# Kernel tuning notes

Measured on AMD Instinct MI355X. Metric: run time of the kernel, lower is better.

The kernel has to match this reference:

```python
import jax, jax.numpy as jnp
import numpy as np

NUM_GRAPHS = 64
NEG_SLOPE = 0.2  # DGL GATConv default negative_slope


def _gat_layer(h, W, a_l, a_r, b, src, dst, n_nodes):
    # DGL GATConv, num_heads=1: feat = h @ W (no bias in fc),
    # e_ij = LeakyReLU(a_l . feat_src + a_r . feat_dst), softmax over incoming
    # edges of each dst node, out_dst = sum alpha * feat_src + bias.
    feat = h @ W                      # [N, D]
    el = feat @ a_l                   # [N]
    er = feat @ a_r                   # [N]
    e = jax.nn.leaky_relu(el[src] + er[dst], NEG_SLOPE)   # [E]
    m = jax.ops.segment_max(e, dst, num_segments=n_nodes)  # per-dst max
    ex = jnp.exp(e - m[dst])
    s = jax.ops.segment_sum(ex, dst, num_segments=n_nodes)
    alpha = ex / s[dst]               # edge softmax
    out = jax.ops.segment_sum(feat[src] * alpha[:, None], dst, num_segments=n_nodes)
    return out + b


def setup_inputs() -> dict:
    key = jax.random.key(0)
    ks = jax.random.split(key, 12)
    N, E, D_IN, D_H, C = 100000, 1600000, 128, 128, 2
    h = jax.random.normal(ks[0], (N, D_IN), dtype=jnp.float32)
    src = jax.random.randint(ks[1], (E,), 0, N)
    dst = jax.random.randint(ks[2], (E,), 0, N)
    graph_id = jnp.sort(jax.random.randint(ks[3], (N,), 0, NUM_GRAPHS))
    sc = 1.0 / np.sqrt(D_IN)
    params = {
        'W1': jax.random.normal(ks[4], (D_IN, D_H), dtype=jnp.float32) * sc,
        'al1': jax.random.normal(ks[5], (D_H,), dtype=jnp.float32) * sc,
        'ar1': jax.random.normal(ks[6], (D_H,), dtype=jnp.float32) * sc,
        'b1': jnp.zeros((D_H,), dtype=jnp.float32),
        'W2': jax.random.normal(ks[7], (D_H, D_H), dtype=jnp.float32) * sc,
        'al2': jax.random.normal(ks[8], (D_H,), dtype=jnp.float32) * sc,
        'ar2': jax.random.normal(ks[9], (D_H,), dtype=jnp.float32) * sc,
        'b2': jnp.zeros((D_H,), dtype=jnp.float32),
        'Wfc': jax.random.normal(ks[10], (D_H, C), dtype=jnp.float32) * sc,
        'bfc': jnp.zeros((C,), dtype=jnp.float32),
    }
    return dict(h=h, src=src, dst=dst, graph_id=graph_id, **params)


def reference(h, src, dst, graph_id, W1, al1, ar1, b1, W2, al2, ar2, b2, Wfc, bfc):
    n_nodes = h.shape[0]
    x = jax.nn.relu(_gat_layer(h, W1, al1, ar1, b1, src, dst, n_nodes))
    x = jax.nn.relu(_gat_layer(x, W2, al2, ar2, b2, src, dst, n_nodes))
    # dgl.mean_nodes over the batched graph
    counts = jax.ops.segment_sum(jnp.ones((n_nodes,), x.dtype), graph_id,
                                 num_segments=NUM_GRAPHS)
    hg = jax.ops.segment_sum(x, graph_id, num_segments=NUM_GRAPHS)
    hg = hg / jnp.clip(counts, 1.0)[:, None]          # [G, D]
    logits = hg @ Wfc + bfc                            # [G, C]
    return jax.nn.log_softmax(logits, axis=-1)
```

## Files before the change

kernel.cpp:

```cpp
#include <hip/hip_runtime.h>
#include <math.h>

#define NUM_GRAPHS 64
#define D 128
#define PCHUNK 16
#define MT 64
#define ETILE 4096

typedef __attribute__((ext_vector_type(8))) short bf16x8;
typedef __attribute__((ext_vector_type(4))) float f32x4;
typedef __attribute__((ext_vector_type(2))) float f32x2;

__device__ __forceinline__ unsigned bf16rne(float x) {
    unsigned u = __float_as_uint(x);
    return (u + 0x7fffu + ((u >> 16) & 1u)) >> 16;
}
__device__ __forceinline__ float bflo(unsigned u) { return __uint_as_float(u << 16); }
__device__ __forceinline__ float bfhi(unsigned u) { return __uint_as_float(u & 0xffff0000u); }

__device__ __forceinline__ unsigned encf(float f) {
    unsigned u = __float_as_uint(f);
    return (u & 0x80000000u) ? ~u : (u | 0x80000000u);
}
__device__ __forceinline__ float decf(unsigned e) {
    unsigned u = (e & 0x80000000u) ? (e & 0x7fffffffu) : ~e;
    return __uint_as_float(u);
}


__global__ __launch_bounds__(256) void k_front(
    const int* __restrict__ dst, int* __restrict__ bhist, int E, int nbT,
    const float* __restrict__ W1, const float* __restrict__ W2,
    unsigned short* __restrict__ Wt1, unsigned short* __restrict__ Wt2,
    const int* __restrict__ gid, int* __restrict__ gs, int* __restrict__ ge, int N) {
    __shared__ int h[1024];
    int b = blockIdx.x;
    int tid = threadIdx.x;
    if (b < nbT) {
        for (int i = tid; i < 1024; i += 256) h[i] = 0;
        __syncthreads();
        int e0 = b * ETILE;
        int e1 = min(e0 + ETILE, E);
        for (int i = e0 + tid; i < e1; i += 256) atomicAdd(&h[dst[i] >> 7], 1);
        __syncthreads();
        for (int i = tid; i < 1024; i += 256)
            if (h[i]) atomicAdd(&bhist[i], h[i]);
    } else if (b < nbT + 16) {
        int bb = b - nbT;
        const float* W = (bb & 8) ? W2 : W1;
        unsigned short* Wt = (bb & 8) ? Wt2 : Wt1;
        int n = (bb & 7) * 16 + (tid >> 4);
        int c = tid & 15;
        unsigned v[8];
        #pragma unroll
        for (int j = 0; j < 8; ++j) v[j] = bf16rne(W[(c * 8 + j) * D + n]);
        uint4 pk;
        pk.x = v[0] | (v[1] << 16);
        pk.y = v[2] | (v[3] << 16);
        pk.z = v[4] | (v[5] << 16);
        pk.w = v[6] | (v[7] << 16);
        ((uint4*)Wt)[n * 16 + c] = pk;
    } else {
        int n = (b - nbT - 16) * 256 + tid;
        if (n >= N) return;
        int g = gid[n];
        if (n == 0 || gid[n - 1] != g) gs[g] = n;
        if (n == N - 1 || gid[n + 1] != g) ge[g] = n;
    }
}

__global__ __launch_bounds__(1024) void k_bucket_scan(const int* __restrict__ bhist,
                                                      int* __restrict__ bbase,
                                                      int* __restrict__ bcur,
                                                      int NB, int E,
                                                      int* __restrict__ row_ptr, int N) {
    __shared__ int sm[1024];
    int t = threadIdx.x;
    int v = (t < NB) ? bhist[t] : 0;
    sm[t] = v;
    __syncthreads();
    for (int off = 1; off < 1024; off <<= 1) {
        int y = (t >= off) ? sm[t - off] : 0;
        __syncthreads();
        sm[t] += y;
        __syncthreads();
    }
    if (t < NB) { bbase[t] = sm[t] - v; bcur[t] = sm[t] - v; }
    if (t == 0) { bbase[NB] = E; row_ptr[N] = E; }
}

__global__ __launch_bounds__(256) void k_partition(const int* __restrict__ src,
                                                   const int* __restrict__ dst,
                                                   int* __restrict__ bcur,
                                                   unsigned* __restrict__ part, int E) {
    __shared__ int h[1024];
    __shared__ int cur[1024];
    int tid = threadIdx.x;
    for (int i = tid; i < 1024; i += 256) h[i] = 0;
    __syncthreads();
    int e0 = blockIdx.x * ETILE;
    int e1 = min(e0 + ETILE, E);
    for (int i = e0 + tid; i < e1; i += 256) atomicAdd(&h[dst[i] >> 7], 1);
    __syncthreads();
    for (int i = tid; i < 1024; i += 256) {
        int c = h[i];
        cur[i] = c ? atomicAdd(&bcur[i], c) : 0;
    }
    __syncthreads();
    for (int i = e0 + tid; i < e1; i += 256) {
        int d = dst[i];
        int b = d >> 7;
        int pos = atomicAdd(&cur[b], 1);
        part[pos] = (unsigned)src[i] | ((unsigned)(d & 127) << 17);
    }
}


__global__ __launch_bounds__(256) void k_gemm_mfma_sort(
    const void* __restrict__ Xv, int x_fp32,
    const unsigned short* __restrict__ Wt16,
    const float* __restrict__ al, const float* __restrict__ ar,
    unsigned short* __restrict__ feat16, float* __restrict__ el,
    float* __restrict__ er, unsigned* __restrict__ glmax_u, int N, int gemmBlocks,
    const unsigned* __restrict__ part, const int* __restrict__ bbase,
    int* __restrict__ row_ptr, int* __restrict__ csr_src) {
    __shared__ uint4 WsU[128 * 16];
    __shared__ uint4 XsU[MT * 16];
    __shared__ float smax[4];
    int bx = blockIdx.x;
    int T = gridDim.x;
    int g0 = (int)((long long)bx * gemmBlocks / T);
    int g1 = (int)((long long)(bx + 1) * gemmBlocks / T);
    int tid = threadIdx.x;

    if (g1 == g0) {
        int b = bx - g0;
        int base = bbase[b];
        int bcnt = bbase[b + 1] - base;
        int* ldeg = (int*)XsU;
        int* lcur = ldeg + 128;
        if (tid < 128) ldeg[tid] = 0;
        __syncthreads();
        for (int i = tid; i < bcnt; i += 256)
            atomicAdd(&ldeg[part[base + i] >> 17], 1);
        __syncthreads();
        int myv = (tid < 128) ? ldeg[tid] : 0;
        for (int off = 1; off < 128; off <<= 1) {
            int y = 0;
            if (tid < 128 && tid >= off) y = ldeg[tid - off];
            __syncthreads();
            if (tid < 128) ldeg[tid] += y;
            __syncthreads();
        }
        if (tid < 128) {
            int excl = ldeg[tid] - myv;
            int node = (b << 7) + tid;
            if (node < N) row_ptr[node] = base + excl;
            lcur[tid] = base + excl;
        }
        __syncthreads();
        for (int i = tid; i < bcnt; i += 256) {
            unsigned v = part[base + i];
            int pos = atomicAdd(&lcur[v >> 17], 1);
            csr_src[pos] = (int)(v & 0x1FFFFu);
        }
        return;
    }

    int row0 = g0 * MT;

    for (int idx = tid; idx < 128 * 16; idx += 256) {
        int n = idx >> 4, c = idx & 15;
        WsU[(n << 4) | (c ^ (n & 15))] = ((const uint4*)Wt16)[idx];
    }
    if (x_fp32) {
        const float4* X4 = (const float4*)Xv;
        for (int idx = tid; idx < MT * 16; idx += 256) {
            int n = idx >> 4, c = idx & 15;
            int row = row0 + n;
            uint4 o = make_uint4(0, 0, 0, 0);
            if (row < N) {
                float4 f0 = X4[(size_t)row * 32 + c * 2];
                float4 f1 = X4[(size_t)row * 32 + c * 2 + 1];
                o.x = bf16rne(f0.x) | (bf16rne(f0.y) << 16);
                o.y = bf16rne(f0.z) | (bf16rne(f0.w) << 16);
                o.z = bf16rne(f1.x) | (bf16rne(f1.y) << 16);
                o.w = bf16rne(f1.z) | (bf16rne(f1.w) << 16);
            }
            XsU[(n << 4) | (c ^ (n & 15))] = o;
        }
    } else {
        const uint4* X16 = (const uint4*)Xv;
        for (int idx = tid; idx < MT * 16; idx += 256) {
            int n = idx >> 4, c = idx & 15;
            int row = row0 + n;
            uint4 o = make_uint4(0, 0, 0, 0);
            if (row < N) o = X16[(size_t)row * 16 + c];
            XsU[(n << 4) | (c ^ (n & 15))] = o;
        }
    }
    __syncthreads();

    int lane = tid & 63, w = tid >> 6;
    int quad = lane >> 4, l16 = lane & 15;
    const bf16x8* WsF = (const bf16x8*)WsU;
    const bf16x8* XsF = (const bf16x8*)XsU;
    f32x4 acc[8];
    #pragma unroll
    for (int i = 0; i < 8; ++i) acc[i] = (f32x4){0.f, 0.f, 0.f, 0.f};

    int arow = w * 16 + l16;
    #pragma unroll
    for (int ks = 0; ks < 4; ++ks) {
        int c = ks * 4 + quad;
        bf16x8 A = XsF[(arow << 4) | (c ^ l16)];
        #pragma unroll
        for (int nt = 0; nt < 8; ++nt) {
            bf16x8 B = WsF[((nt * 16 + l16) << 4) | (c ^ l16)];
            acc[nt] = __builtin_amdgcn_mfma_f32_16x16x32_bf16(A, B, acc[nt], 0, 0, 0);
        }
    }

    float alv[8], arv[8];
    #pragma unroll
    for (int nt = 0; nt < 8; ++nt) { alv[nt] = al[nt * 16 + l16]; arv[nt] = ar[nt * 16 + l16]; }
    float lmax = -1e30f;
    #pragma unroll
    for (int r = 0; r < 4; ++r) {
        float pl = 0.f, pr = 0.f;
        #pragma unroll
        for (int nt = 0; nt < 8; ++nt) { pl += acc[nt][r] * alv[nt]; pr += acc[nt][r] * arv[nt]; }
        #pragma unroll
        for (int o = 1; o < 16; o <<= 1) { pl += __shfl_xor(pl, o); pr += __shfl_xor(pr, o); }
        int row = row0 + w * 16 + quad * 4 + r;
        if (l16 == 0 && row < N) { el[row] = pl; er[row] = pr; }
        lmax = fmaxf(lmax, pl);
    }
    lmax = fmaxf(lmax, __shfl_xor(lmax, 16));
    lmax = fmaxf(lmax, __shfl_xor(lmax, 32));
    if (lane == 0) smax[w] = lmax;

    unsigned short* XsS = (unsigned short*)XsU;
    #pragma unroll
    for (int nt = 0; nt < 8; ++nt)
        #pragma unroll
        for (int r = 0; r < 4; ++r) {
            int lrow = w * 16 + quad * 4 + r;
            int col = nt * 16 + l16;
            int ch = col >> 3;
            int sc = ch ^ (lrow & 15);
            XsS[lrow * 128 + sc * 8 + (col & 7)] = (unsigned short)bf16rne(acc[nt][r]);
        }
    __syncthreads();
    if (tid == 0) {
        float bm = fmaxf(fmaxf(smax[0], smax[1]), fmaxf(smax[2], smax[3]));
        atomicMax(glmax_u, encf(bm));
    }
    for (int idx = tid; idx < MT * 16; idx += 256) {
        int n = idx >> 4, c = idx & 15;
        int row = row0 + n;
        if (row < N) ((uint4*)feat16)[(size_t)row * 16 + c] = XsU[(n << 4) | (c ^ (n & 15))];
    }
}


__global__ __launch_bounds__(256) void k_aggregate(
    const unsigned short* __restrict__ feat16, const float* __restrict__ el,
    const float* __restrict__ er, const int* __restrict__ row_ptr,
    const int* __restrict__ csr_src, const float* __restrict__ bias,
    const unsigned* __restrict__ glmax_u, unsigned short* __restrict__ outv, int N) {
    int wid = (blockIdx.x * blockDim.x + threadIdx.x) >> 6;
    int lane = threadIdx.x & 63;
    if (wid >= N) return;
    int beg = row_ptr[wid], end = row_ptr[wid + 1];
    float erd = er[wid];
    float M = decf(glmax_u[0]) + erd;
    M = fmaxf(M, 0.2f * M);

    int qa = lane >> 4, sub = lane & 15;
    const char* fb = (const char*)feat16 + (sub << 4);
    f32x2 a0 = {0.f, 0.f}, a1 = {0.f, 0.f}, a2 = {0.f, 0.f}, a3 = {0.f, 0.f};
    float s = 0.f;
    int j = beg + qa;
    for (; j + 12 < end; j += 16) {
        int sn0 = csr_src[j], sn1 = csr_src[j + 4];
        int sn2 = csr_src[j + 8], sn3 = csr_src[j + 12];
        float t0 = el[sn0] + erd, t1 = el[sn1] + erd;
        float t2 = el[sn2] + erd, t3 = el[sn3] + erd;
        uint4 q0 = *(const uint4*)(fb + ((unsigned)sn0 << 8));
        uint4 q1 = *(const uint4*)(fb + ((unsigned)sn1 << 8));
        uint4 q2 = *(const uint4*)(fb + ((unsigned)sn2 << 8));
        uint4 q3 = *(const uint4*)(fb + ((unsigned)sn3 << 8));
        t0 = fmaxf(t0, 0.2f * t0); t1 = fmaxf(t1, 0.2f * t1);
        t2 = fmaxf(t2, 0.2f * t2); t3 = fmaxf(t3, 0.2f * t3);
        float w0 = __expf(t0 - M), w1 = __expf(t1 - M);
        float w2 = __expf(t2 - M), w3 = __expf(t3 - M);
        s += (w0 + w1) + (w2 + w3);
        f32x2 f;
        f.x = bflo(q0.x); f.y = bfhi(q0.x); a0 += w0 * f;
        f.x = bflo(q0.y); f.y = bfhi(q0.y); a1 += w0 * f;
        f.x = bflo(q0.z); f.y = bfhi(q0.z); a2 += w0 * f;
        f.x = bflo(q0.w); f.y = bfhi(q0.w); a3 += w0 * f;
        f.x = bflo(q1.x); f.y = bfhi(q1.x); a0 += w1 * f;
        f.x = bflo(q1.y); f.y = bfhi(q1.y); a1 += w1 * f;
        f.x = bflo(q1.z); f.y = bfhi(q1.z); a2 += w1 * f;
        f.x = bflo(q1.w); f.y = bfhi(q1.w); a3 += w1 * f;
        f.x = bflo(q2.x); f.y = bfhi(q2.x); a0 += w2 * f;
        f.x = bflo(q2.y); f.y = bfhi(q2.y); a1 += w2 * f;
        f.x = bflo(q2.z); f.y = bfhi(q2.z); a2 += w2 * f;
        f.x = bflo(q2.w); f.y = bfhi(q2.w); a3 += w2 * f;
        f.x = bflo(q3.x); f.y = bfhi(q3.x); a0 += w3 * f;
        f.x = bflo(q3.y); f.y = bfhi(q3.y); a1 += w3 * f;
        f.x = bflo(q3.z); f.y = bfhi(q3.z); a2 += w3 * f;
        f.x = bflo(q3.w); f.y = bfhi(q3.w); a3 += w3 * f;
    }
    for (; j + 4 < end; j += 8) {
        int sn0 = csr_src[j], sn1 = csr_src[j + 4];
        float t0 = el[sn0] + erd, t1 = el[sn1] + erd;
        uint4 q0 = *(const uint4*)(fb + ((unsigned)sn0 << 8));
        uint4 q1 = *(const uint4*)(fb + ((unsigned)sn1 << 8));
        t0 = fmaxf(t0, 0.2f * t0); t1 = fmaxf(t1, 0.2f * t1);
        float w0 = __expf(t0 - M), w1 = __expf(t1 - M);
        s += w0 + w1;
        f32x2 f;
        f.x = bflo(q0.x); f.y = bfhi(q0.x); a0 += w0 * f;
        f.x = bflo(q0.y); f.y = bfhi(q0.y); a1 += w0 * f;
        f.x = bflo(q0.z); f.y = bfhi(q0.z); a2 += w0 * f;
        f.x = bflo(q0.w); f.y = bfhi(q0.w); a3 += w0 * f;
        f.x = bflo(q1.x); f.y = bfhi(q1.x); a0 += w1 * f;
        f.x = bflo(q1.y); f.y = bfhi(q1.y); a1 += w1 * f;
        f.x = bflo(q1.z); f.y = bfhi(q1.z); a2 += w1 * f;
        f.x = bflo(q1.w); f.y = bfhi(q1.w); a3 += w1 * f;
    }
    if (j < end) {
        int sn = csr_src[j];
        float t = el[sn] + erd;
        uint4 q = *(const uint4*)(fb + ((unsigned)sn << 8));
        t = fmaxf(t, 0.2f * t);
        float w = __expf(t - M);
        s += w;
        f32x2 f;
        f.x = bflo(q.x); f.y = bfhi(q.x); a0 += w * f;
        f.x = bflo(q.y); f.y = bfhi(q.y); a1 += w * f;
        f.x = bflo(q.z); f.y = bfhi(q.z); a2 += w * f;
        f.x = bflo(q.w); f.y = bfhi(q.w); a3 += w * f;
    }
    float vr[8] = {a0.x, a0.y, a1.x, a1.y, a2.x, a2.y, a3.x, a3.y};
    #pragma unroll
    for (int c = 0; c < 8; ++c) {
        vr[c] += __shfl_xor(vr[c], 16);
        vr[c] += __shfl_xor(vr[c], 32);
    }
    s += __shfl_xor(s, 16);
    s += __shfl_xor(s, 32);
    float inv = (end > beg) ? 1.f / s : 0.f;
    if (lane < 16) {
        float4 b0 = ((const float4*)bias)[lane * 2];
        float4 b1 = ((const float4*)bias)[lane * 2 + 1];
        float v[8];
        v[0] = fmaxf(vr[0] * inv + b0.x, 0.f);
        v[1] = fmaxf(vr[1] * inv + b0.y, 0.f);
        v[2] = fmaxf(vr[2] * inv + b0.z, 0.f);
        v[3] = fmaxf(vr[3] * inv + b0.w, 0.f);
        v[4] = fmaxf(vr[4] * inv + b1.x, 0.f);
        v[5] = fmaxf(vr[5] * inv + b1.y, 0.f);
        v[6] = fmaxf(vr[6] * inv + b1.z, 0.f);
        v[7] = fmaxf(vr[7] * inv + b1.w, 0.f);
        uint4 pk;
        pk.x = bf16rne(v[0]) | (bf16rne(v[1]) << 16);
        pk.y = bf16rne(v[2]) | (bf16rne(v[3]) << 16);
        pk.z = bf16rne(v[4]) | (bf16rne(v[5]) << 16);
        pk.w = bf16rne(v[6]) | (bf16rne(v[7]) << 16);
        ((uint4*)outv)[(size_t)wid * 16 + lane] = pk;
    }
}


__global__ __launch_bounds__(256) void k_pool_partial(const unsigned short* __restrict__ x,
                                                      const int* __restrict__ gs,
                                                      const int* __restrict__ ge,
                                                      float* __restrict__ hg) {
    int g = blockIdx.x, c = blockIdx.y;
    int start = gs[g], last = ge[g];
    if (start > last) return;
    int sub = threadIdx.x & 15;
    int r   = threadIdx.x >> 4;
    const uint4* x4 = (const uint4*)x;
    float acc[8] = {};
    for (int n = start + c * 16 + r; n <= last; n += PCHUNK * 16) {
        uint4 q = x4[(size_t)n * 16 + sub];
        acc[0] += bflo(q.x); acc[1] += bfhi(q.x);
        acc[2] += bflo(q.y); acc[3] += bfhi(q.y);
        acc[4] += bflo(q.z); acc[5] += bfhi(q.z);
        acc[6] += bflo(q.w); acc[7] += bfhi(q.w);
    }
    __shared__ float sm[256][8];
    #pragma unroll
    for (int k = 0; k < 8; ++k) sm[threadIdx.x][k] = acc[k];
    __syncthreads();
    for (int off = 8; off >= 1; off >>= 1) {
        if (r < off) {
            #pragma unroll
            for (int k = 0; k < 8; ++k)
                sm[threadIdx.x][k] += sm[threadIdx.x + off * 16][k];
        }
        __syncthreads();
    }
    if (r == 0) {
        #pragma unroll
        for (int k = 0; k < 8; ++k)
            atomicAdd(&hg[g * D + sub * 8 + k], sm[sub][k]);
    }
}

__global__ void k_final(const float* __restrict__ hg, const int* __restrict__ gs,
                        const int* __restrict__ ge, const float* __restrict__ Wfc,
                        const float* __restrict__ bfc, float* __restrict__ out) {
    int g = threadIdx.x;
    if (g >= NUM_GRAPHS) return;
    int start = gs[g], last = ge[g];
    float cnt = (start <= last) ? (float)(last - start + 1) : 1.f;
    float ic = 1.f / cnt;
    float l0 = bfc[0], l1 = bfc[1];
    for (int d = 0; d < D; d++) {
        float v = hg[g * D + d] * ic;
        l0 += v * Wfc[2 * d];
        l1 += v * Wfc[2 * d + 1];
    }
    float mm = fmaxf(l0, l1);
    float lse = mm + logf(expf(l0 - mm) + expf(l1 - mm));
    out[2 * g] = l0 - lse;
    out[2 * g + 1] = l1 - lse;
}


extern "C" void kernel_launch(void* const* d_in, const int* in_sizes, int n_in,
                              void* d_out, int out_size, void* d_ws, size_t ws_size,
                              hipStream_t stream) {
    const float* h   = (const float*)d_in[0];
    const int* src   = (const int*)d_in[1];
    const int* dst   = (const int*)d_in[2];
    const int* gid   = (const int*)d_in[3];
    const float* W1  = (const float*)d_in[4];
    const float* al1 = (const float*)d_in[5];
    const float* ar1 = (const float*)d_in[6];
    const float* b1  = (const float*)d_in[7];
    const float* W2  = (const float*)d_in[8];
    const float* al2 = (const float*)d_in[9];
    const float* ar2 = (const float*)d_in[10];
    const float* b2  = (const float*)d_in[11];
    const float* Wfc = (const float*)d_in[12];
    const float* bfc = (const float*)d_in[13];
    float* out = (float*)d_out;

    int N = in_sizes[0] / D;
    int E = in_sizes[1];
    int NB = (N + 127) >> 7;

    char* p = (char*)d_ws;
    unsigned short* feat16  = (unsigned short*)p; p += (size_t)N * D * 2;
    unsigned short* featAgg = (unsigned short*)p; p += (size_t)N * D * 2;
    float* el    = (float*)p; p += (size_t)N * 4;
    float* er    = (float*)p; p += (size_t)N * 4;
    int* row_ptr = (int*)p;   p += (size_t)(N + 4) * 4;
    int* csr_src = (int*)p;   p += (size_t)E * 4;
    unsigned* part = (unsigned*)p; p += (size_t)E * 4;
    int* bhist   = (int*)p;   p += 1028 * 4;
    unsigned* glmaxu = (unsigned*)p; p += 4 * 4;
    float* hg    = (float*)p; p += NUM_GRAPHS * D * 4;
    size_t zbytes = (char*)p - (char*)bhist;
    int* bbase   = (int*)p;   p += 1028 * 4;
    int* bcur    = (int*)p;   p += 1028 * 4;
    int* gs      = (int*)p;   p += NUM_GRAPHS * 4;
    int* ge      = (int*)p;   p += NUM_GRAPHS * 4;
    unsigned short* Wt1 = (unsigned short*)p; p += D * D * 2;
    unsigned short* Wt2 = (unsigned short*)p; p += D * D * 2;

    int nbN = (N + 255) / 256;
    int nbW = (N * 64 + 255) / 256;
    int nbT = (E + ETILE - 1) / ETILE;
    int gemmB = (N + MT - 1) / MT;

    hipMemsetAsync(bhist, 0, zbytes, stream);
    hipMemsetAsync(gs, 0x7f, NUM_GRAPHS * 4, stream);
    hipMemsetAsync(ge, 0xff, NUM_GRAPHS * 4, stream);

    k_front<<<nbT + 16 + nbN, 256, 0, stream>>>(dst, bhist, E, nbT,
                                                W1, W2, Wt1, Wt2, gid, gs, ge, N);
    k_bucket_scan<<<1, 1024, 0, stream>>>(bhist, bbase, bcur, NB, E, row_ptr, N);
    k_partition<<<nbT, 256, 0, stream>>>(src, dst, bcur, part, E);

    k_gemm_mfma_sort<<<gemmB + NB, 256, 0, stream>>>(
        h, 1, Wt1, al1, ar1, feat16, el, er, glmaxu, N, gemmB,
        part, bbase, row_ptr, csr_src);
    k_aggregate<<<nbW, 256, 0, stream>>>(feat16, el, er, row_ptr, csr_src,
                                         b1, glmaxu, featAgg, N);

    k_gemm_mfma_sort<<<gemmB, 256, 0, stream>>>(
        featAgg, 0, Wt2, al2, ar2, feat16, el, er, glmaxu + 1, N, gemmB,
        part, bbase, row_ptr, csr_src);
    k_aggregate<<<nbW, 256, 0, stream>>>(feat16, el, er, row_ptr, csr_src,
                                         b2, glmaxu + 1, featAgg, N);

    k_pool_partial<<<dim3(NUM_GRAPHS, PCHUNK), 256, 0, stream>>>(featAgg, gs, ge, hg);
    k_final<<<1, 64, 0, stream>>>(hg, gs, ge, Wfc, bfc, out);
}
```

Measured before the change: 355.9 us.

## Precompute edge softmax weights and inverse sums in a separate per-bucket kernel

Adds a k_weights kernel that computes the exp attention weight for each edge in CSR order into a buffer, and accumulates per-destination inverse sums with shared-memory atomics, once per 128-node bucket. The aggregate kernel then reads these precomputed weights instead of gathering el and running exp per edge, and the csr array now stores packed src|dst-local values. The aim is to take the random el gather and transcendental work out of the latency-bound gather loop. In exchange it adds an extra kernel launch and an extra E-sized write and read of the weight buffer per layer. The shared-atomic summation order also differs from the previous per-lane sums.

```diff
diff --git a/kernel.cpp b/kernel.cpp
--- a/kernel.cpp
+++ b/kernel.cpp
@@ -123,7 +123,7 @@
     unsigned short* __restrict__ feat16, float* __restrict__ el,
     float* __restrict__ er, unsigned* __restrict__ glmax_u, int N, int gemmBlocks,
     const unsigned* __restrict__ part, const int* __restrict__ bbase,
-    int* __restrict__ row_ptr, int* __restrict__ csr_src) {
+    int* __restrict__ row_ptr, unsigned* __restrict__ csr_src) {
     __shared__ uint4 WsU[128 * 16];
     __shared__ uint4 XsU[MT * 16];
     __shared__ float smax[4];
@@ -162,7 +162,7 @@
         for (int i = tid; i < bcnt; i += 256) {
             unsigned v = part[base + i];
             int pos = atomicAdd(&lcur[v >> 17], 1);
-            csr_src[pos] = (int)(v & 0x1FFFFu);
+            csr_src[pos] = v;
         }
         return;
     }
@@ -264,38 +264,64 @@
 }
 
 
+__global__ __launch_bounds__(256) void k_weights(
+    const unsigned* __restrict__ csr_packed, const int* __restrict__ bbase,
+    const float* __restrict__ el, const float* __restrict__ er,
+    const unsigned* __restrict__ glmax_u, float* __restrict__ wbuf,
+    float* __restrict__ sinv, int N) {
+    __shared__ float sl[128];
+    int b = blockIdx.x;
+    int base = bbase[b], endq = bbase[b + 1];
+    int tid = threadIdx.x;
+    if (tid < 128) sl[tid] = 0.f;
+    __syncthreads();
+    float EL = decf(glmax_u[0]);
+    for (int i = base + tid; i < endq; i += 256) {
+        unsigned v = csr_packed[i];
+        int sn = v & 0x1FFFFu;
+        int dl = v >> 17;
+        float erd = er[(b << 7) + dl];
+        float M = EL + erd; M = fmaxf(M, 0.2f * M);
+        float t = el[sn] + erd; t = fmaxf(t, 0.2f * t);
+        float w = __expf(t - M);
+        wbuf[i] = w;
+        atomicAdd(&sl[dl], w);
+    }
+    __syncthreads();
+    if (tid < 128) {
+        int node = (b << 7) + tid;
+        if (node < N) {
+            float s = sl[tid];
+            sinv[node] = s > 0.f ? 1.f / s : 0.f;
+        }
+    }
+}
+
+
 __global__ __launch_bounds__(256) void k_aggregate(
-    const unsigned short* __restrict__ feat16, const float* __restrict__ el,
-    const float* __restrict__ er, const int* __restrict__ row_ptr,
-    const int* __restrict__ csr_src, const float* __restrict__ bias,
-    const unsigned* __restrict__ glmax_u, unsigned short* __restrict__ outv, int N) {
+    const unsigned short* __restrict__ feat16,
+    const unsigned* __restrict__ csr_packed, const float* __restrict__ wbuf,
+    const float* __restrict__ sinv, const int* __restrict__ row_ptr,
+    const float* __restrict__ bias, unsigned short* __restrict__ outv, int N) {
     int wid = (blockIdx.x * blockDim.x + threadIdx.x) >> 6;
     int lane = threadIdx.x & 63;
     if (wid >= N) return;
     int beg = row_ptr[wid], end = row_ptr[wid + 1];
-    float erd = er[wid];
-    float M = decf(glmax_u[0]) + erd;
-    M = fmaxf(M, 0.2f * M);
+    float si = sinv[wid];
 
     int qa = lane >> 4, sub = lane & 15;
     const char* fb = (const char*)feat16 + (sub << 4);
     f32x2 a0 = {0.f, 0.f}, a1 = {0.f, 0.f}, a2 = {0.f, 0.f}, a3 = {0.f, 0.f};
-    float s = 0.f;
     int j = beg + qa;
     for (; j + 12 < end; j += 16) {
-        int sn0 = csr_src[j], sn1 = csr_src[j + 4];
-        int sn2 = csr_src[j + 8], sn3 = csr_src[j + 12];
-        float t0 = el[sn0] + erd, t1 = el[sn1] + erd;
-        float t2 = el[sn2] + erd, t3 = el[sn3] + erd;
-        uint4 q0 = *(const uint4*)(fb + ((unsigned)sn0 << 8));
-        uint4 q1 = *(const uint4*)(fb + ((unsigned)sn1 << 8));
-        uint4 q2 = *(const uint4*)(fb + ((unsigned)sn2 << 8));
-        uint4 q3 = *(const uint4*)(fb + ((unsigned)sn3 << 8));
-        t0 = fmaxf(t0, 0.2f * t0); t1 = fmaxf(t1, 0.2f * t1);
-        t2 = fmaxf(t2, 0.2f * t2); t3 = fmaxf(t3, 0.2f * t3);
-        float w0 = __expf(t0 - M), w1 = __expf(t1 - M);
-        float w2 = __expf(t2 - M), w3 = __expf(t3 - M);
-        s += (w0 + w1) + (w2 + w3);
+        unsigned v0 = csr_packed[j], v1 = csr_packed[j + 4];
+        unsigned v2 = csr_packed[j + 8], v3 = csr_packed[j + 12];
+        float w0 = wbuf[j], w1 = wbuf[j + 4];
+        float w2 = wbuf[j + 8], w3 = wbuf[j + 12];
+        uint4 q0 = *(const uint4*)(fb + ((v0 & 0x1FFFFu) << 8));
+        uint4 q1 = *(const uint4*)(fb + ((v1 & 0x1FFFFu) << 8));
+        uint4 q2 = *(const uint4*)(fb + ((v2 & 0x1FFFFu) << 8));
+        uint4 q3 = *(const uint4*)(fb + ((v3 & 0x1FFFFu) << 8));
         f32x2 f;
         f.x = bflo(q0.x); f.y = bfhi(q0.x); a0 += w0 * f;
         f.x = bflo(q0.y); f.y = bfhi(q0.y); a1 += w0 * f;
@@ -314,31 +340,10 @@
         f.x = bflo(q3.z); f.y = bfhi(q3.z); a2 += w3 * f;
         f.x = bflo(q3.w); f.y = bfhi(q3.w); a3 += w3 * f;
     }
-    for (; j + 4 < end; j += 8) {
-        int sn0 = csr_src[j], sn1 = csr_src[j + 4];
-        float t0 = el[sn0] + erd, t1 = el[sn1] + erd;
-        uint4 q0 = *(const uint4*)(fb + ((unsigned)sn0 << 8));
-        uint4 q1 = *(const uint4*)(fb + ((unsigned)sn1 << 8));
-        t0 = fmaxf(t0, 0.2f * t0); t1 = fmaxf(t1, 0.2f * t1);
-        float w0 = __expf(t0 - M), w1 = __expf(t1 - M);
-        s += w0 + w1;
-        f32x2 f;
-        f.x = bflo(q0.x); f.y = bfhi(q0.x); a0 += w0 * f;
-        f.x = bflo(q0.y); f.y = bfhi(q0.y); a1 += w0 * f;
-        f.x = bflo(q0.z); f.y = bfhi(q0.z); a2 += w0 * f;
-        f.x = bflo(q0.w); f.y = bfhi(q0.w); a3 += w0 * f;
-        f.x = bflo(q1.x); f.y = bfhi(q1.x); a0 += w1 * f;
-        f.x = bflo(q1.y); f.y = bfhi(q1.y); a1 += w1 * f;
-        f.x = bflo(q1.z); f.y = bfhi(q1.z); a2 += w1 * f;
-        f.x = bflo(q1.w); f.y = bfhi(q1.w); a3 += w1 * f;
-    }
-    if (j < end) {
-        int sn = csr_src[j];
-        float t = el[sn] + erd;
-        uint4 q = *(const uint4*)(fb + ((unsigned)sn << 8));
-        t = fmaxf(t, 0.2f * t);
-        float w = __expf(t - M);
-        s += w;
+    for (; j < end; j += 4) {
+        unsigned v = csr_packed[j];
+        float w = wbuf[j];
+        uint4 q = *(const uint4*)(fb + ((v & 0x1FFFFu) << 8));
         f32x2 f;
         f.x = bflo(q.x); f.y = bfhi(q.x); a0 += w * f;
         f.x = bflo(q.y); f.y = bfhi(q.y); a1 += w * f;
@@ -351,21 +356,18 @@
         vr[c] += __shfl_xor(vr[c], 16);
         vr[c] += __shfl_xor(vr[c], 32);
     }
-    s += __shfl_xor(s, 16);
-    s += __shfl_xor(s, 32);
-    float inv = (end > beg) ? 1.f / s : 0.f;
     if (lane < 16) {
         float4 b0 = ((const float4*)bias)[lane * 2];
         float4 b1 = ((const float4*)bias)[lane * 2 + 1];
         float v[8];
-        v[0] = fmaxf(vr[0] * inv + b0.x, 0.f);
-        v[1] = fmaxf(vr[1] * inv + b0.y, 0.f);
-        v[2] = fmaxf(vr[2] * inv + b0.z, 0.f);
-        v[3] = fmaxf(vr[3] * inv + b0.w, 0.f);
-        v[4] = fmaxf(vr[4] * inv + b1.x, 0.f);
-        v[5] = fmaxf(vr[5] * inv + b1.y, 0.f);
-        v[6] = fmaxf(vr[6] * inv + b1.z, 0.f);
-        v[7] = fmaxf(vr[7] * inv + b1.w, 0.f);
+        v[0] = fmaxf(vr[0] * si + b0.x, 0.f);
+        v[1] = fmaxf(vr[1] * si + b0.y, 0.f);
+        v[2] = fmaxf(vr[2] * si + b0.z, 0.f);
+        v[3] = fmaxf(vr[3] * si + b0.w, 0.f);
+        v[4] = fmaxf(vr[4] * si + b1.x, 0.f);
+        v[5] = fmaxf(vr[5] * si + b1.y, 0.f);
+        v[6] = fmaxf(vr[6] * si + b1.z, 0.f);
+        v[7] = fmaxf(vr[7] * si + b1.w, 0.f);
         uint4 pk;
         pk.x = bf16rne(v[0]) | (bf16rne(v[1]) << 16);
         pk.y = bf16rne(v[2]) | (bf16rne(v[3]) << 16);
@@ -462,9 +464,11 @@
     unsigned short* featAgg = (unsigned short*)p; p += (size_t)N * D * 2;
     float* el    = (float*)p; p += (size_t)N * 4;
     float* er    = (float*)p; p += (size_t)N * 4;
+    float* sinv  = (float*)p; p += (size_t)N * 4;
     int* row_ptr = (int*)p;   p += (size_t)(N + 4) * 4;
-    int* csr_src = (int*)p;   p += (size_t)E * 4;
+    unsigned* csr_src = (unsigned*)p; p += (size_t)E * 4;
     unsigned* part = (unsigned*)p; p += (size_t)E * 4;
+    float* wbuf  = (float*)p; p += (size_t)E * 4;
     int* bhist   = (int*)p;   p += 1028 * 4;
     unsigned* glmaxu = (unsigned*)p; p += 4 * 4;
     float* hg    = (float*)p; p += NUM_GRAPHS * D * 4;
@@ -493,14 +497,16 @@
     k_gemm_mfma_sort<<<gemmB + NB, 256, 0, stream>>>(
         h, 1, Wt1, al1, ar1, feat16, el, er, glmaxu, N, gemmB,
         part, bbase, row_ptr, csr_src);
-    k_aggregate<<<nbW, 256, 0, stream>>>(feat16, el, er, row_ptr, csr_src,
-                                         b1, glmaxu, featAgg, N);
+    k_weights<<<NB, 256, 0, stream>>>(csr_src, bbase, el, er, glmaxu, wbuf, sinv, N);
+    k_aggregate<<<nbW, 256, 0, stream>>>(feat16, csr_src, wbuf, sinv, row_ptr,
+                                         b1, featAgg, N);
 
     k_gemm_mfma_sort<<<gemmB, 256, 0, stream>>>(
         featAgg, 0, Wt2, al2, ar2, feat16, el, er, glmaxu + 1, N, gemmB,
         part, bbase, row_ptr, csr_src);
-    k_aggregate<<<nbW, 256, 0, stream>>>(feat16, el, er, row_ptr, csr_src,
-                                         b2, glmaxu + 1, featAgg, N);
+    k_weights<<<NB, 256, 0, stream>>>(csr_src, bbase, el, er, glmaxu + 1, wbuf, sinv, N);
+    k_aggregate<<<nbW, 256, 0, stream>>>(feat16, csr_src, wbuf, sinv, row_ptr,
+                                         b2, featAgg, N);
 
     k_pool_partial<<<dim3(NUM_GRAPHS, PCHUNK), 256, 0, stream>>>(featAgg, gs, ge, hg);
     k_final<<<1, 64, 0, stream>>>(hg, gs, ge, Wfc, bfc, out);
```

Result: slower. 392.9 us (+10.4%).

## Fuse mean-node pooling into second GAT aggregation with replicated atomic accumulators

Applied to the files above, without the earlier changes.

The second aggregate kernel now scales each node's output by the inverse node count of its graph. It reduces the four nodes of a block in shared memory and atomically adds the result into one of 16 replicated per-graph accumulators, instead of writing bf16 features and running a separate pooling kernel. Inverse counts are computed in the scan kernel, and the final kernel sums the replicas before the classifier. This removes a full feature write and re-read plus one launch, at the cost of many global float atomics with possible contention on sorted graph ids.

```diff
diff --git a/kernel.cpp b/kernel.cpp
--- a/kernel.cpp
+++ b/kernel.cpp
@@ -3,9 +3,9 @@
 
 #define NUM_GRAPHS 64
 #define D 128
-#define PCHUNK 16
 #define MT 64
 #define ETILE 4096
+#define NREP 16
 
 typedef __attribute__((ext_vector_type(8))) short bf16x8;
 typedef __attribute__((ext_vector_type(4))) float f32x4;
@@ -73,7 +73,10 @@
                                                       int* __restrict__ bbase,
                                                       int* __restrict__ bcur,
                                                       int NB, int E,
-                                                      int* __restrict__ row_ptr, int N) {
+                                                      int* __restrict__ row_ptr, int N,
+                                                      const int* __restrict__ gs,
+                                                      const int* __restrict__ ge,
+                                                      float* __restrict__ ginv) {
     __shared__ int sm[1024];
     int t = threadIdx.x;
     int v = (t < NB) ? bhist[t] : 0;
@@ -87,6 +90,10 @@
     }
     if (t < NB) { bbase[t] = sm[t] - v; bcur[t] = sm[t] - v; }
     if (t == 0) { bbase[NB] = E; row_ptr[N] = E; }
+    if (t < NUM_GRAPHS) {
+        int s = gs[t], e = ge[t];
+        ginv[t] = (s <= e) ? 1.f / (float)(e - s + 1) : 0.f;
+    }
 }
 
 __global__ __launch_bounds__(256) void k_partition(const int* __restrict__ src,
@@ -264,173 +271,187 @@
 }
 
 
+template <bool POOL>
 __global__ __launch_bounds__(256) void k_aggregate(
     const unsigned short* __restrict__ feat16, const float* __restrict__ el,
     const float* __restrict__ er, const int* __restrict__ row_ptr,
     const int* __restrict__ csr_src, const float* __restrict__ bias,
-    const unsigned* __restrict__ glmax_u, unsigned short* __restrict__ outv, int N) {
-    int wid = (blockIdx.x * blockDim.x + threadIdx.x) >> 6;
-    int lane = threadIdx.x & 63;
-    if (wid >= N) return;
-    int beg = row_ptr[wid], end = row_ptr[wid + 1];
-    float erd = er[wid];
-    float M = decf(glmax_u[0]) + erd;
-    M = fmaxf(M, 0.2f * M);
-
-    int qa = lane >> 4, sub = lane & 15;
-    const char* fb = (const char*)feat16 + (sub << 4);
-    f32x2 a0 = {0.f, 0.f}, a1 = {0.f, 0.f}, a2 = {0.f, 0.f}, a3 = {0.f, 0.f};
-    float s = 0.f;
-    int j = beg + qa;
-    for (; j + 12 < end; j += 16) {
-        int sn0 = csr_src[j], sn1 = csr_src[j + 4];
-        int sn2 = csr_src[j + 8], sn3 = csr_src[j + 12];
-        float t0 = el[sn0] + erd, t1 = el[sn1] + erd;
-        float t2 = el[sn2] + erd, t3 = el[sn3] + erd;
-        uint4 q0 = *(const uint4*)(fb + ((unsigned)sn0 << 8));
-        uint4 q1 = *(const uint4*)(fb + ((unsigned)sn1 << 8));
-        uint4 q2 = *(const uint4*)(fb + ((unsigned)sn2 << 8));
-        uint4 q3 = *(const uint4*)(fb + ((unsigned)sn3 << 8));
-        t0 = fmaxf(t0, 0.2f * t0); t1 = fmaxf(t1, 0.2f * t1);
-        t2 = fmaxf(t2, 0.2f * t2); t3 = fmaxf(t3, 0.2f * t3);
-        float w0 = __expf(t0 - M), w1 = __expf(t1 - M);
-        float w2 = __expf(t2 - M), w3 = __expf(t3 - M);
-        s += (w0 + w1) + (w2 + w3);
-        f32x2 f;
-        f.x = bflo(q0.x); f.y = bfhi(q0.x); a0 += w0 * f;
-        f.x = bflo(q0.y); f.y = bfhi(q0.y); a1 += w0 * f;
-        f.x = bflo(q0.z); f.y = bfhi(q0.z); a2 += w0 * f;
-        f.x = bflo(q0.w); f.y = bfhi(q0.w); a3 += w0 * f;
-        f.x = bflo(q1.x); f.y = bfhi(q1.x); a0 += w1 * f;
-        f.x = bflo(q1.y); f.y = bfhi(q1.y); a1 += w1 * f;
-        f.x = bflo(q1.z); f.y = bfhi(q1.z); a2 += w1 * f;
-        f.x = bflo(q1.w); f.y = bfhi(q1.w); a3 += w1 * f;
-        f.x = bflo(q2.x); f.y = bfhi(q2.x); a0 += w2 * f;
-        f.x = bflo(q2.y); f.y = bfhi(q2.y); a1 += w2 * f;
-        f.x = bflo(q2.z); f.y = bfhi(q2.z); a2 += w2 * f;
-        f.x = bflo(q2.w); f.y = bfhi(q2.w); a3 += w2 * f;
-        f.x = bflo(q3.x); f.y = bfhi(q3.x); a0 += w3 * f;
-        f.x = bflo(q3.y); f.y = bfhi(q3.y); a1 += w3 * f;
-        f.x = bflo(q3.z); f.y = bfhi(q3.z); a2 += w3 * f;
-        f.x = bflo(q3.w); f.y = bfhi(q3.w); a3 += w3 * f;
-    }
-    for (; j + 4 < end; j += 8) {
-        int sn0 = csr_src[j], sn1 = csr_src[j + 4];
-        float t0 = el[sn0] + erd, t1 = el[sn1] + erd;
-        uint4 q0 = *(const uint4*)(fb + ((unsigned)sn0 << 8));
-        uint4 q1 = *(const uint4*)(fb + ((unsigned)sn1 << 8));
-        t0 = fmaxf(t0, 0.2f * t0); t1 = fmaxf(t1, 0.2f * t1);
-        float w0 = __expf(t0 - M), w1 = __expf(t1 - M);
-        s += w0 + w1;
-        f32x2 f;
-        f.x = bflo(q0.x); f.y = bfhi(q0.x); a0 += w0 * f;
-        f.x = bflo(q0.y); f.y = bfhi(q0.y); a1 += w0 * f;
-        f.x = bflo(q0.z); f.y = bfhi(q0.z); a2 += w0 * f;
-        f.x = bflo(q0.w); f.y = bfhi(q0.w); a3 += w0 * f;
-        f.x = bflo(q1.x); f.y = bfhi(q1.x); a0 += w1 * f;
-        f.x = bflo(q1.y); f.y = bfhi(q1.y); a1 += w1 * f;
-        f.x = bflo(q1.z); f.y = bfhi(q1.z); a2 += w1 * f;
-        f.x = bflo(q1.w); f.y = bfhi(q1.w); a3 += w1 * f;
-    }
-    if (j < end) {
-        int sn = csr_src[j];
-        float t = el[sn] + erd;
-        uint4 q = *(const uint4*)(fb + ((unsigned)sn << 8));
-        t = fmaxf(t, 0.2f * t);
-        float w = __expf(t - M);
-        s += w;
-        f32x2 f;
-        f.x = bflo(q.x); f.y = bfhi(q.x); a0 += w * f;
-        f.x = bflo(q.y); f.y = bfhi(q.y); a1 += w * f;
-        f.x = bflo(q.z); f.y = bfhi(q.z); a2 += w * f;
-        f.x = bflo(q.w); f.y = bfhi(q.w); a3 += w * f;
-    }
-    float vr[8] = {a0.x, a0.y, a1.x, a1.y, a2.x, a2.y, a3.x, a3.y};
-    #pragma unroll
-    for (int c = 0; c < 8; ++c) {
-        vr[c] += __shfl_xor(vr[c], 16);
-        vr[c] += __shfl_xor(vr[c], 32);
-    }
-    s += __shfl_xor(s, 16);
-    s += __shfl_xor(s, 32);
-    float inv = (end > beg) ? 1.f / s : 0.f;
-    if (lane < 16) {
-        float4 b0 = ((const float4*)bias)[lane * 2];
-        float4 b1 = ((const float4*)bias)[lane * 2 + 1];
-        float v[8];
-        v[0] = fmaxf(vr[0] * inv + b0.x, 0.f);
-        v[1] = fmaxf(vr[1] * inv + b0.y, 0.f);
-        v[2] = fmaxf(vr[2] * inv + b0.z, 0.f);
-        v[3] = fmaxf(vr[3] * inv + b0.w, 0.f);
-        v[4] = fmaxf(vr[4] * inv + b1.x, 0.f);
-        v[5] = fmaxf(vr[5] * inv + b1.y, 0.f);
-        v[6] = fmaxf(vr[6] * inv + b1.z, 0.f);
-        v[7] = fmaxf(vr[7] * inv + b1.w, 0.f);
-        uint4 pk;
-        pk.x = bf16rne(v[0]) | (bf16rne(v[1]) << 16);
-        pk.y = bf16rne(v[2]) | (bf16rne(v[3]) << 16);
-        pk.z = bf16rne(v[4]) | (bf16rne(v[5]) << 16);
-        pk.w = bf16rne(v[6]) | (bf16rne(v[7]) << 16);
-        ((uint4*)outv)[(size_t)wid * 16 + lane] = pk;
-    }
-}
-
-
-__global__ __launch_bounds__(256) void k_pool_partial(const unsigned short* __restrict__ x,
-                                                      const int* __restrict__ gs,
-                                                      const int* __restrict__ ge,
-                                                      float* __restrict__ hg) {
-    int g = blockIdx.x, c = blockIdx.y;
-    int start = gs[g], last = ge[g];
-    if (start > last) return;
-    int sub = threadIdx.x & 15;
-    int r   = threadIdx.x >> 4;
-    const uint4* x4 = (const uint4*)x;
-    float acc[8] = {};
-    for (int n = start + c * 16 + r; n <= last; n += PCHUNK * 16) {
-        uint4 q = x4[(size_t)n * 16 + sub];
-        acc[0] += bflo(q.x); acc[1] += bfhi(q.x);
-        acc[2] += bflo(q.y); acc[3] += bfhi(q.y);
-        acc[4] += bflo(q.z); acc[5] += bfhi(q.z);
-        acc[6] += bflo(q.w); acc[7] += bfhi(q.w);
-    }
-    __shared__ float sm[256][8];
-    #pragma unroll
-    for (int k = 0; k < 8; ++k) sm[threadIdx.x][k] = acc[k];
-    __syncthreads();
-    for (int off = 8; off >= 1; off >>= 1) {
-        if (r < off) {
+    const unsigned* __restrict__ glmax_u, unsigned short* __restrict__ outv,
+    const int* __restrict__ gid, const float* __restrict__ ginv,
+    float* __restrict__ hgrep, int N) {
+    int tid = threadIdx.x;
+    int wid = (blockIdx.x * blockDim.x + tid) >> 6;
+    int lane = tid & 63;
+    int w = tid >> 6;
+    bool active = wid < N;
+    if (!POOL && !active) return;
+
+    float v[8];
+    int g = 0;
+    float ic = 0.f;
+    if (active) {
+        int beg = row_ptr[wid], end = row_ptr[wid + 1];
+        float erd = er[wid];
+        float M = decf(glmax_u[0]) + erd;
+        M = fmaxf(M, 0.2f * M);
+
+        int qa = lane >> 4, sub = lane & 15;
+        const char* fb = (const char*)feat16 + (sub << 4);
+        f32x2 a0 = {0.f, 0.f}, a1 = {0.f, 0.f}, a2 = {0.f, 0.f}, a3 = {0.f, 0.f};
+        float s = 0.f;
+        int j = beg + qa;
+        for (; j + 12 < end; j += 16) {
+            int sn0 = csr_src[j], sn1 = csr_src[j + 4];
+            int sn2 = csr_src[j + 8], sn3 = csr_src[j + 12];
+            float t0 = el[sn0] + erd, t1 = el[sn1] + erd;
+            float t2 = el[sn2] + erd, t3 = el[sn3] + erd;
+            uint4 q0 = *(const uint4*)(fb + ((unsigned)sn0 << 8));
+            uint4 q1 = *(const uint4*)(fb + ((unsigned)sn1 << 8));
+            uint4 q2 = *(const uint4*)(fb + ((unsigned)sn2 << 8));
+            uint4 q3 = *(const uint4*)(fb + ((unsigned)sn3 << 8));
+            t0 = fmaxf(t0, 0.2f * t0); t1 = fmaxf(t1, 0.2f * t1);
+            t2 = fmaxf(t2, 0.2f * t2); t3 = fmaxf(t3, 0.2f * t3);
+            float w0 = __expf(t0 - M), w1 = __expf(t1 - M);
+            float w2 = __expf(t2 - M), w3 = __expf(t3 - M);
+            s += (w0 + w1) + (w2 + w3);
+            f32x2 f;
+            f.x = bflo(q0.x); f.y = bfhi(q0.x); a0 += w0 * f;
+            f.x = bflo(q0.y); f.y = bfhi(q0.y); a1 += w0 * f;
+            f.x = bflo(q0.z); f.y = bfhi(q0.z); a2 += w0 * f;
+            f.x = bflo(q0.w); f.y = bfhi(q0.w); a3 += w0 * f;
+            f.x = bflo(q1.x); f.y = bfhi(q1.x); a0 += w1 * f;
+            f.x = bflo(q1.y); f.y = bfhi(q1.y); a1 += w1 * f;
+            f.x = bflo(q1.z); f.y = bfhi(q1.z); a2 += w1 * f;
+            f.x = bflo(q1.w); f.y = bfhi(q1.w); a3 += w1 * f;
+            f.x = bflo(q2.x); f.y = bfhi(q2.x); a0 += w2 * f;
+            f.x = bflo(q2.y); f.y = bfhi(q2.y); a1 += w2 * f;
+            f.x = bflo(q2.z); f.y = bfhi(q2.z); a2 += w2 * f;
+            f.x = bflo(q2.w); f.y = bfhi(q2.w); a3 += w2 * f;
+            f.x = bflo(q3.x); f.y = bfhi(q3.x); a0 += w3 * f;
+            f.x = bflo(q3.y); f.y = bfhi(q3.y); a1 += w3 * f;
+            f.x = bflo(q3.z); f.y = bfhi(q3.z); a2 += w3 * f;
+            f.x = bflo(q3.w); f.y = bfhi(q3.w); a3 += w3 * f;
+        }
+        for (; j + 4 < end; j += 8) {
+            int sn0 = csr_src[j], sn1 = csr_src[j + 4];
+            float t0 = el[sn0] + erd, t1 = el[sn1] + erd;
+            uint4 q0 = *(const uint4*)(fb + ((unsigned)sn0 << 8));
+            uint4 q1 = *(const uint4*)(fb + ((unsigned)sn1 << 8));
+            t0 = fmaxf(t0, 0.2f * t0); t1 = fmaxf(t1, 0.2f * t1);
+            float w0 = __expf(t0 - M), w1 = __expf(t1 - M);
+            s += w0 + w1;
+            f32x2 f;
+            f.x = bflo(q0.x); f.y = bfhi(q0.x); a0 += w0 * f;
+            f.x = bflo(q0.y); f.y = bfhi(q0.y); a1 += w0 * f;
+            f.x = bflo(q0.z); f.y = bfhi(q0.z); a2 += w0 * f;
+            f.x = bflo(q0.w); f.y = bfhi(q0.w); a3 += w0 * f;
+            f.x = bflo(q1.x); f.y = bfhi(q1.x); a0 += w1 * f;
+            f.x = bflo(q1.y); f.y = bfhi(q1.y); a1 += w1 * f;
+            f.x = bflo(q1.z); f.y = bfhi(q1.z); a2 += w1 * f;
+            f.x = bflo(q1.w); f.y = bfhi(q1.w); a3 += w1 * f;
+        }
+        if (j < end) {
+            int sn = csr_src[j];
+            float t = el[sn] + erd;
+            uint4 q = *(const uint4*)(fb + ((unsigned)sn << 8));
+            t = fmaxf(t, 0.2f * t);
+            float wq = __expf(t - M);
+            s += wq;
+            f32x2 f;
+            f.x = bflo(q.x); f.y = bfhi(q.x); a0 += wq * f;
+            f.x = bflo(q.y); f.y = bfhi(q.y); a1 += wq * f;
+            f.x = bflo(q.z); f.y = bfhi(q.z); a2 += wq * f;
+            f.x = bflo(q.w); f.y = bfhi(q.w); a3 += wq * f;
+        }
+        float vr[8] = {a0.x, a0.y, a1.x, a1.y, a2.x, a2.y, a3.x, a3.y};
+        #pragma unroll
+        for (int c = 0; c < 8; ++c) {
+            vr[c] += __shfl_xor(vr[c], 16);
+            vr[c] += __shfl_xor(vr[c], 32);
+        }
+        s += __shfl_xor(s, 16);
+        s += __shfl_xor(s, 32);
+        float inv = (end > beg) ? 1.f / s : 0.f;
+        if (lane < 16) {
+            float4 b0 = ((const float4*)bias)[lane * 2];
+            float4 b1 = ((const float4*)bias)[lane * 2 + 1];
+            v[0] = fmaxf(vr[0] * inv + b0.x, 0.f);
+            v[1] = fmaxf(vr[1] * inv + b0.y, 0.f);
+            v[2] = fmaxf(vr[2] * inv + b0.z, 0.f);
+            v[3] = fmaxf(vr[3] * inv + b0.w, 0.f);
+            v[4] = fmaxf(vr[4] * inv + b1.x, 0.f);
+            v[5] = fmaxf(vr[5] * inv + b1.y, 0.f);
+            v[6] = fmaxf(vr[6] * inv + b1.z, 0.f);
+            v[7] = fmaxf(vr[7] * inv + b1.w, 0.f);
+        }
+        if (POOL) { g = gid[wid]; ic = ginv[g]; }
+    }
+
+    if (POOL) {
+        __shared__ float smp[4][128];
+        __shared__ int sgr[4];
+        if (lane < 16) {
             #pragma unroll
             for (int k = 0; k < 8; ++k)
-                sm[threadIdx.x][k] += sm[threadIdx.x + off * 16][k];
-        }
-        __syncthreads();
-    }
-    if (r == 0) {
-        #pragma unroll
-        for (int k = 0; k < 8; ++k)
-            atomicAdd(&hg[g * D + sub * 8 + k], sm[sub][k]);
-    }
-}
-
-__global__ void k_final(const float* __restrict__ hg, const int* __restrict__ gs,
-                        const int* __restrict__ ge, const float* __restrict__ Wfc,
-                        const float* __restrict__ bfc, float* __restrict__ out) {
-    int g = threadIdx.x;
-    if (g >= NUM_GRAPHS) return;
-    int start = gs[g], last = ge[g];
-    float cnt = (start <= last) ? (float)(last - start + 1) : 1.f;
-    float ic = 1.f / cnt;
-    float l0 = bfc[0], l1 = bfc[1];
-    for (int d = 0; d < D; d++) {
-        float v = hg[g * D + d] * ic;
-        l0 += v * Wfc[2 * d];
-        l1 += v * Wfc[2 * d + 1];
-    }
-    float mm = fmaxf(l0, l1);
-    float lse = mm + logf(expf(l0 - mm) + expf(l1 - mm));
-    out[2 * g] = l0 - lse;
-    out[2 * g + 1] = l1 - lse;
+                smp[w][lane * 8 + k] = active ? v[k] * ic : 0.f;
+        }
+        if (lane == 0) sgr[w] = active ? g : -1;
+        __syncthreads();
+        if (tid < 128) {
+            int rep = (int)(blockIdx.x & (NREP - 1));
+            float* hb = hgrep + (size_t)rep * NUM_GRAPHS * D + tid;
+            int gprev = -1; float sacc = 0.f;
+            #pragma unroll
+            for (int ww = 0; ww < 4; ++ww) {
+                int gg = sgr[ww];
+                if (gg < 0) continue;
+                float val = smp[ww][tid];
+                if (gg == gprev) sacc += val;
+                else {
+                    if (gprev >= 0) atomicAdd(hb + gprev * D, sacc);
+                    gprev = gg; sacc = val;
+                }
+            }
+            if (gprev >= 0) atomicAdd(hb + gprev * D, sacc);
+        }
+    } else {
+        if (lane < 16) {
+            uint4 pk;
+            pk.x = bf16rne(v[0]) | (bf16rne(v[1]) << 16);
+            pk.y = bf16rne(v[2]) | (bf16rne(v[3]) << 16);
+            pk.z = bf16rne(v[4]) | (bf16rne(v[5]) << 16);
+            pk.w = bf16rne(v[6]) | (bf16rne(v[7]) << 16);
+            ((uint4*)outv)[(size_t)wid * 16 + lane] = pk;
+        }
+    }
+}
+
+
+__global__ __launch_bounds__(256) void k_final(const float* __restrict__ hgrep,
+                                               const float* __restrict__ Wfc,
+                                               const float* __restrict__ bfc,
+                                               float* __restrict__ out) {
+    __shared__ float hgs[NUM_GRAPHS * D];
+    int tid = threadIdx.x;
+    for (int i = tid; i < NUM_GRAPHS * D; i += 256) {
+        float v = 0.f;
+        #pragma unroll
+        for (int r = 0; r < NREP; ++r) v += hgrep[(size_t)r * NUM_GRAPHS * D + i];
+        hgs[i] = v;
+    }
+    __syncthreads();
+    if (tid < NUM_GRAPHS) {
+        float l0 = bfc[0], l1 = bfc[1];
+        for (int d = 0; d < D; d++) {
+            float v = hgs[tid * D + d];
+            l0 += v * Wfc[2 * d];
+            l1 += v * Wfc[2 * d + 1];
+        }
+        float mm = fmaxf(l0, l1);
+        float lse = mm + logf(expf(l0 - mm) + expf(l1 - mm));
+        out[2 * tid] = l0 - lse;
+        out[2 * tid + 1] = l1 - lse;
+    }
 }
 
 
@@ -467,12 +488,13 @@
     unsigned* part = (unsigned*)p; p += (size_t)E * 4;
     int* bhist   = (int*)p;   p += 1028 * 4;
     unsigned* glmaxu = (unsigned*)p; p += 4 * 4;
-    float* hg    = (float*)p; p += NUM_GRAPHS * D * 4;
+    float* hgrep = (float*)p; p += (size_t)NREP * NUM_GRAPHS * D * 4;
     size_t zbytes = (char*)p - (char*)bhist;
     int* bbase   = (int*)p;   p += 1028 * 4;
     int* bcur    = (int*)p;   p += 1028 * 4;
     int* gs      = (int*)p;   p += NUM_GRAPHS * 4;
     int* ge      = (int*)p;   p += NUM_GRAPHS * 4;
+    float* ginv  = (float*)p; p += NUM_GRAPHS * 4;
     unsigned short* Wt1 = (unsigned short*)p; p += D * D * 2;
     unsigned short* Wt2 = (unsigned short*)p; p += D * D * 2;
 
@@ -487,21 +509,23 @@
 
     k_front<<<nbT + 16 + nbN, 256, 0, stream>>>(dst, bhist, E, nbT,
                                                 W1, W2, Wt1, Wt2, gid, gs, ge, N);
-    k_bucket_scan<<<1, 1024, 0, stream>>>(bhist, bbase, bcur, NB, E, row_ptr, N);
+    k_bucket_scan<<<1, 1024, 0, stream>>>(bhist, bbase, bcur, NB, E, row_ptr, N,
+                                          gs, ge, ginv);
     k_partition<<<nbT, 256, 0, stream>>>(src, dst, bcur, part, E);
 
     k_gemm_mfma_sort<<<gemmB + NB, 256, 0, stream>>>(
         h, 1, Wt1, al1, ar1, feat16, el, er, glmaxu, N, gemmB,
         part, bbase, row_ptr, csr_src);
-    k_aggregate<<<nbW, 256, 0, stream>>>(feat16, el, er, row_ptr, csr_src,
-                                         b1, glmaxu, featAgg, N);
+    k_aggregate<false><<<nbW, 256, 0, stream>>>(feat16, el, er, row_ptr, csr_src,
+                                                b1, glmaxu, featAgg,
+                                                gid, ginv, hgrep, N);
 
     k_gemm_mfma_sort<<<gemmB, 256, 0, stream>>>(
         featAgg, 0, Wt2, al2, ar2, feat16, el, er, glmaxu + 1, N, gemmB,
         part, bbase, row_ptr, csr_src);
-    k_aggregate<<<nbW, 256, 0, stream>>>(feat16, el, er, row_ptr, csr_src,
-                                         b2, glmaxu + 1, featAgg, N);
-
-    k_pool_partial<<<dim3(NUM_GRAPHS, PCHUNK), 256, 0, stream>>>(featAgg, gs, ge, hg);
-    k_final<<<1, 64, 0, stream>>>(hg, gs, ge, Wfc, bfc, out);
-}
+    k_aggregate<true><<<nbW, 256, 0, stream>>>(feat16, el, er, row_ptr, csr_src,
+                                               b2, glmaxu + 1, (unsigned short*)0,
+                                               gid, ginv, hgrep, N);
+
+    k_final<<<1, 256, 0, stream>>>(hgrep, Wfc, bfc, out);
+}
```

New measurement: 394.3 us. 1.11x slower.
